# Kernel tuning notes

Hardware: AMD Instinct MI355X
Metric: run time of the kernel (lower is better)

The kernel has to match this reference:

```python
import jax, jax.numpy as jnp
import numpy as np

# Model dims
B, N, T = 2, 32, 256
D_MODEL = 128          # d_slow
D_STATE = 16
N_LAYERS = 2
EXPAND = 2
D_INNER = EXPAND * D_MODEL   # 256
D_CONV = 4
DT_RANK = (D_MODEL + 15) // 16  # 8


def setup_inputs() -> dict:
    key = jax.random.key(0)
    ks = jax.random.split(key, 8)
    s = lambda k, shape, scale: jax.random.normal(k, shape, jnp.float32) * scale
    return {
        "x": jax.random.normal(ks[0], (B, N, T, D_MODEL), jnp.float32),
        "in_proj_w": s(ks[1], (N_LAYERS, D_MODEL, 2 * D_INNER), 0.05),
        "conv_w": s(ks[2], (N_LAYERS, D_INNER, 1, D_CONV), 0.2),   # depthwise conv kernels
        "conv_b": jnp.zeros((N_LAYERS, D_INNER), jnp.float32),
        "x_proj_w": s(ks[3], (N_LAYERS, D_INNER, DT_RANK + 2 * D_STATE), 0.05),
        "dt_proj_w": s(ks[4], (N_LAYERS, DT_RANK, D_INNER), 0.1),
        "dt_proj_b": jnp.full((N_LAYERS, D_INNER), -4.0, jnp.float32),  # softplus(-4) ~ small dt
        # slow-timescale init: A_log = log(U(0.001, 0.1)) so A = -exp(A_log) is a weak decay
        "A_log": jnp.log(jax.random.uniform(ks[5], (N_LAYERS, D_INNER, D_STATE),
                                            minval=1e-3, maxval=0.1)),
        "D_param": jnp.ones((N_LAYERS, D_INNER), jnp.float32),
        "out_proj_w": s(ks[6], (N_LAYERS, D_INNER, D_MODEL), 0.05),
    }


def _selective_scan(u, delta, A, Bm, Cm, Dp):
    # u, delta: [b, t, d]; A: [d, n]; Bm, Cm: [b, t, n]; Dp: [d]
    deltaA = jnp.exp(jnp.einsum('btd,dn->btdn', delta, A))          # [b,t,d,n]
    deltaBu = jnp.einsum('btd,btn->btdn', delta * u, Bm)            # [b,t,d,n]
    # time-major for scan
    dA_t = jnp.transpose(deltaA, (1, 0, 2, 3))
    dBu_t = jnp.transpose(deltaBu, (1, 0, 2, 3))
    c_t = jnp.transpose(Cm, (1, 0, 2))

    def step(h, xs):
        dA, dBu, c = xs
        h = dA * h + dBu                                            # [b,d,n]
        y = jnp.einsum('bdn,bn->bd', h, c)
        return h, y

    h0 = jnp.zeros(u.shape[:1] + (u.shape[-1], A.shape[-1]), u.dtype)
    _, ys = jax.lax.scan(step, h0, (dA_t, dBu_t, c_t))              # ys: [t,b,d]
    y = jnp.transpose(ys, (1, 0, 2))
    return y + u * Dp


def _mamba_block(h, in_w, cw, cb, xw, dtw, dtb, A_log, Dp, ow):
    # h: [b, t, d_model]
    xz = h @ in_w                                                   # [b,t,2*d_inner]
    u, res = jnp.split(xz, 2, axis=-1)
    # causal depthwise conv over time
    u_nch = jnp.transpose(u, (0, 2, 1))                             # [b,d_inner,t]
    u_conv = jax.lax.conv_general_dilated(
        u_nch, cw, window_strides=(1,), padding=[(D_CONV - 1, 0)],
        dimension_numbers=('NCH', 'OIH', 'NCH'), feature_group_count=D_INNER)
    u = jax.nn.silu(jnp.transpose(u_conv + cb[None, :, None], (0, 2, 1)))
    # input-dependent dt, B, C
    dbl = u @ xw                                                    # [b,t,dt_rank+2n]
    dt, Bm, Cm = jnp.split(dbl, [DT_RANK, DT_RANK + D_STATE], axis=-1)
    delta = jax.nn.softplus(dt @ dtw + dtb)                         # [b,t,d_inner]
    A = -jnp.exp(A_log)                                             # [d_inner, n]
    y = _selective_scan(u, delta, A, Bm, Cm, Dp)
    return (y * jax.nn.silu(res)) @ ow


def reference(x, in_proj_w, conv_w, conv_b, x_proj_w, dt_proj_w, dt_proj_b,
              A_log, D_param, out_proj_w):
    b, n, t, d = x.shape
    h = x.reshape(b * n, t, d)
    for l in range(N_LAYERS):
        h = _mamba_block(h, in_proj_w[l], conv_w[l], conv_b[l], x_proj_w[l],
                         dt_proj_w[l], dt_proj_b[l], A_log[l], D_param[l],
                         out_proj_w[l])
    return h.reshape(b, n, t, d)
```

## Files before the change

### kernel.cpp

```cpp
#include <hip/hip_runtime.h>
#include <math.h>

#define BT 64
#define T 256
#define DM 128
#define DI 256
#define DS 16
#define DR 8
#define M_ROWS (BT*T)
#define NC 16
#define CL (T/NC)
#define SSZ (BT*DI*DS)

typedef __attribute__((ext_vector_type(8))) short short8v;
typedef __attribute__((ext_vector_type(4))) float f32x4;
typedef __attribute__((ext_vector_type(4))) unsigned int uint4v;
union U8 { unsigned int u[4]; uint4v v; short8v s; };

__device__ __forceinline__ float fast_silu(float x) {
  return x * __builtin_amdgcn_rcpf(1.0f + __expf(-x));
}
__device__ __forceinline__ float softplus_f(float x) {
  return fmaxf(x, 0.0f) + __logf(1.0f + __expf(-fabsf(x)));
}

__device__ __forceinline__ void split3(const float* x, short8v& o1, short8v& o2, short8v& o3) {
  unsigned int h1[8], h2[8], h3[8];
#pragma unroll
  for (int e = 0; e < 8; e++) {
    const float xe = x[e];
    const unsigned int a = __float_as_uint(xe) & 0xFFFF0000u;
    const float r1 = xe - __uint_as_float(a);
    const unsigned int b = __float_as_uint(r1) & 0xFFFF0000u;
    const float r2 = r1 - __uint_as_float(b);
    const unsigned int c = __float_as_uint(r2) & 0xFFFF0000u;
    h1[e] = a; h2[e] = b; h3[e] = c;
  }
  U8 u1, u2, u3;
#pragma unroll
  for (int q = 0; q < 4; q++) {
    u1.u[q] = (h1[2 * q] >> 16) | (h1[2 * q + 1] & 0xFFFF0000u);
    u2.u[q] = (h2[2 * q] >> 16) | (h2[2 * q + 1] & 0xFFFF0000u);
    u3.u[q] = (h3[2 * q] >> 16) | (h3[2 * q + 1] & 0xFFFF0000u);
  }
  o1 = u1.s; o2 = u2.s; o3 = u3.s;
}

__global__ __launch_bounds__(64) void prep_all(
    const float* __restrict__ in_w, const float* __restrict__ xw,
    const float* __restrict__ dtw, const float* __restrict__ ow,
    unsigned int* __restrict__ pw1, unsigned int* __restrict__ pwb,
    unsigned int* __restrict__ pow_) {
  const int b = blockIdx.x;
  const int l = threadIdx.x;
  const int rA = l & 15, kg = l >> 4;
  float x[8];
  unsigned int* dst;
  size_t base;
  if (b < 256) {
    const int layer = b >> 7, rem = b & 127;
    const int ks = rem >> 5, cf = rem & 31;
    const int col = cf * 16 + rA, k0 = ks * 32 + kg * 8;
    const float* W = in_w + (size_t)layer * 128 * 512;
#pragma unroll
    for (int e = 0; e < 8; e++) x[e] = W[(size_t)(k0 + e) * 512 + col];
    dst = pw1 + (size_t)layer * 98304;
    base = (((size_t)ks * 32 + cf) * 64 + l) * 4;
    short8v p1, p2, p3; split3(x, p1, p2, p3);
    U8 t;
    t.s = p1; *reinterpret_cast<uint4v*>(dst + base) = t.v;
    t.s = p2; *reinterpret_cast<uint4v*>(dst + 32768 + base) = t.v;
    t.s = p3; *reinterpret_cast<uint4v*>(dst + 65536 + base) = t.v;
  } else if (b < 576) {
    const int bb = b - 256;
    const int layer = bb / 160, rem = bb % 160;
    const int ks = rem / 20, cf = rem % 20;
    const int col = cf * 16 + rA, k0 = ks * 32 + kg * 8;
    const float* xwl = xw + (size_t)layer * DI * 40;
    const float* dtwl = dtw + (size_t)layer * DR * DI;
#pragma unroll
    for (int e = 0; e < 8; e++) {
      const int k = k0 + e;
      float v = 0.f;
      if (col < 256) {
#pragma unroll
        for (int r = 0; r < DR; r++) v += xwl[k * 40 + r] * dtwl[r * DI + col];
      } else if (col < 288) {
        v = xwl[k * 40 + 8 + (col - 256)];
      }
      x[e] = v;
    }
    dst = pwb + (size_t)layer * 122880;
    base = (((size_t)ks * 20 + cf) * 64 + l) * 4;
    short8v p1, p2, p3; split3(x, p1, p2, p3);
    U8 t;
    t.s = p1; *reinterpret_cast<uint4v*>(dst + base) = t.v;
    t.s = p2; *reinterpret_cast<uint4v*>(dst + 40960 + base) = t.v;
    t.s = p3; *reinterpret_cast<uint4v*>(dst + 81920 + base) = t.v;
  } else {
    const int bb = b - 576;
    const int layer = bb >> 6, rem = bb & 63;
    const int ks = rem >> 3, cf = rem & 7;
    const int col = cf * 16 + rA, k0 = ks * 32 + kg * 8;
    const float* W = ow + (size_t)layer * 256 * 128;
#pragma unroll
    for (int e = 0; e < 8; e++) x[e] = W[(size_t)(k0 + e) * 128 + col];
    dst = pow_ + (size_t)layer * 49152;
    base = (((size_t)ks * 8 + cf) * 64 + l) * 4;
    short8v p1, p2, p3; split3(x, p1, p2, p3);
    U8 t;
    t.s = p1; *reinterpret_cast<uint4v*>(dst + base) = t.v;
    t.s = p2; *reinterpret_cast<uint4v*>(dst + 16384 + base) = t.v;
    t.s = p3; *reinterpret_cast<uint4v*>(dst + 32768 + base) = t.v;
  }
}

template <int FR, int CF, int EPI>
__global__ __launch_bounds__(256, 4) void gemm_mfma(
    const float* __restrict__ Af, const unsigned int* __restrict__ Bp,
    float* __restrict__ C, float* __restrict__ Bb, float* __restrict__ Cb,
    const float* __restrict__ dtb, int M, int Nn, int K, int cpx) {
  const int NWC = Nn / (16 * CF);
  const int tile = (blockIdx.x & 7) * cpx + (blockIdx.x >> 3);
  const int wid = tile * 4 + (threadIdx.x >> 6);
  const int l = threadIdx.x & 63;
  const int mw = wid / NWC, nw = wid % NWC;
  const int wr0 = mw * (16 * FR), wc0 = nw * (16 * CF);
  const int rA = l & 15, kg = l >> 4;
  const int NF = Nn / 16, Kt = K >> 5;

  f32x4 acc[FR][CF];
#pragma unroll
  for (int fr = 0; fr < FR; fr++)
#pragma unroll
    for (int j = 0; j < CF; j++) acc[fr][j] = (f32x4){0.f, 0.f, 0.f, 0.f};

  for (int ks = 0; ks < Kt; ks++) {
    short8v bf[3][CF];
#pragma unroll
    for (int p = 0; p < 3; p++)
#pragma unroll
      for (int j = 0; j < CF; j++) {
        U8 t;
        t.v = *reinterpret_cast<const uint4v*>(
            Bp + ((((size_t)p * Kt + ks) * NF + (wc0 >> 4) + j) * 64 + l) * 4);
        bf[p][j] = t.s;
      }
#pragma unroll
    for (int fr = 0; fr < FR; fr++) {
      const float* ap = Af + (size_t)(wr0 + fr * 16 + rA) * K + ks * 32 + kg * 8;
      float x[8];
      *reinterpret_cast<float4*>(x) = *reinterpret_cast<const float4*>(ap);
      *reinterpret_cast<float4*>(x + 4) = *reinterpret_cast<const float4*>(ap + 4);
      short8v a1, a2, a3;
      split3(x, a1, a2, a3);
#pragma unroll
      for (int j = 0; j < CF; j++) {
        f32x4 c = acc[fr][j];
        c = __builtin_amdgcn_mfma_f32_16x16x32_bf16(a1, bf[0][j], c, 0, 0, 0);
        c = __builtin_amdgcn_mfma_f32_16x16x32_bf16(a1, bf[1][j], c, 0, 0, 0);
        c = __builtin_amdgcn_mfma_f32_16x16x32_bf16(a2, bf[0][j], c, 0, 0, 0);
        c = __builtin_amdgcn_mfma_f32_16x16x32_bf16(a1, bf[2][j], c, 0, 0, 0);
        c = __builtin_amdgcn_mfma_f32_16x16x32_bf16(a3, bf[0][j], c, 0, 0, 0);
        c = __builtin_amdgcn_mfma_f32_16x16x32_bf16(a2, bf[1][j], c, 0, 0, 0);
        acc[fr][j] = c;
      }
    }
  }

  const int cr = (l >> 4) * 4;
  const int cc = l & 15;
  if (EPI == 0) {
#pragma unroll
    for (int fr = 0; fr < FR; fr++)
#pragma unroll
      for (int j = 0; j < CF; j++) {
        const int col = wc0 + j * 16 + cc;
#pragma unroll
        for (int r = 0; r < 4; r++)
          C[(size_t)(wr0 + fr * 16 + cr + r) * Nn + col] = acc[fr][j][r];
      }
  } else if (EPI == 1) {
#pragma unroll
    for (int fr = 0; fr < FR; fr++)
#pragma unroll
      for (int j = 0; j < CF; j++) {
        const int col = wc0 + j * 16 + cc;
        if (col < 256) {
          const float bias = dtb[col];
#pragma unroll
          for (int r = 0; r < 4; r++)
            C[(size_t)(wr0 + fr * 16 + cr + r) * DI + col] =
                softplus_f(acc[fr][j][r] + bias);
        } else if (col < 272) {
#pragma unroll
          for (int r = 0; r < 4; r++)
            Bb[(size_t)(wr0 + fr * 16 + cr + r) * DS + (col - 256)] = acc[fr][j][r];
        } else if (col < 288) {
#pragma unroll
          for (int r = 0; r < 4; r++)
            Cb[(size_t)(wr0 + fr * 16 + cr + r) * DS + (col - 272)] = acc[fr][j][r];
        }
      }
  } else {
#pragma unroll
    for (int fr = 0; fr < FR; fr++)
#pragma unroll
      for (int j = 0; j < CF; j++) {
        const int col = wc0 + j * 16 + cc;
        if (col < 256) {
#pragma unroll
          for (int r = 0; r < 4; r++)
            C[(size_t)(wr0 + fr * 16 + cr + r) * Nn + col] = acc[fr][j][r];
        } else {
#pragma unroll
          for (int r = 0; r < 4; r++)
            C[(size_t)(wr0 + fr * 16 + cr + r) * Nn + col] = fast_silu(acc[fr][j][r]);
        }
      }
  }
}

__global__ __launch_bounds__(256) void conv_silu_kernel(
    const float* __restrict__ xzr,
    const float* __restrict__ cw, const float* __restrict__ cb,
    float* __restrict__ u) {
  const int d = threadIdx.x;
  const int m0 = blockIdx.x * 8;
  const int t0 = m0 & (T - 1);
  const float4 cv = *reinterpret_cast<const float4*>(&cw[d * 4]);
  const float bias = cb[d];
  float w0 = 0.f, w1 = 0.f, w2 = 0.f;
  if (t0 != 0) {
    w0 = xzr[(size_t)(m0 - 3) * 512 + d];
    w1 = xzr[(size_t)(m0 - 2) * 512 + d];
    w2 = xzr[(size_t)(m0 - 1) * 512 + d];
  }
#pragma unroll
  for (int i = 0; i < 8; i++) {
    const size_t m = m0 + i;
    const float cur = xzr[m * 512 + d];
    const float a = bias + cv.x * w0 + cv.y * w1 + cv.z * w2 + cv.w * cur;
    u[m * DI + d] = fast_silu(a);
    w0 = w1; w1 = w2; w2 = cur;
  }
}

__global__ __launch_bounds__(256) void scan_phase1(
    const float* __restrict__ delta, const float* __restrict__ u,
    const float* __restrict__ Bb, const float* __restrict__ A_log,
    float* __restrict__ Pb, float* __restrict__ H) {
  const int c  = blockIdx.x;
  const int bt = blockIdx.y;
  const int d  = threadIdx.x;

  float An[16];
  const float4* al = reinterpret_cast<const float4*>(&A_log[d * DS]);
#pragma unroll
  for (int q = 0; q < 4; q++) {
    float4 a = al[q];
    An[q * 4 + 0] = -__expf(a.x);
    An[q * 4 + 1] = -__expf(a.y);
    An[q * 4 + 2] = -__expf(a.z);
    An[q * 4 + 3] = -__expf(a.w);
  }

  float h[16];
#pragma unroll
  for (int n = 0; n < 16; n++) h[n] = 0.f;
  float Sdl = 0.f;

  const size_t m0 = (size_t)bt * T + c * CL;
  for (int t = 0; t < CL; t++) {
    const size_t m = m0 + t;
    const float dl = delta[m * DI + d];
    const float uu = u[m * DI + d];
    const float du = dl * uu;
    Sdl += dl;
    const float4* bp = reinterpret_cast<const float4*>(&Bb[m * DS]);
    const float4 B0 = bp[0], B1 = bp[1], B2 = bp[2], B3 = bp[3];
    const float Bv[16] = {B0.x, B0.y, B0.z, B0.w, B1.x, B1.y, B1.z, B1.w,
                          B2.x, B2.y, B2.z, B2.w, B3.x, B3.y, B3.z, B3.w};
#pragma unroll
    for (int n = 0; n < 16; n++) {
      const float dA = __expf(dl * An[n]);
      h[n] = dA * h[n] + du * Bv[n];
    }
  }

  const size_t idx = ((size_t)c * BT + bt) * 4096 + (size_t)d * 16;
#pragma unroll
  for (int q = 0; q < 4; q++) {
    float4 hv = {h[q * 4 + 0], h[q * 4 + 1], h[q * 4 + 2], h[q * 4 + 3]};
    *reinterpret_cast<float4*>(&H[idx + q * 4]) = hv;
  }
#pragma unroll
  for (int q = 0; q < 4; q++) {
    float4 pv = {__expf(An[q * 4 + 0] * Sdl), __expf(An[q * 4 + 1] * Sdl),
                 __expf(An[q * 4 + 2] * Sdl), __expf(An[q * 4 + 3] * Sdl)};
    *reinterpret_cast<float4*>(&Pb[idx + q * 4]) = pv;
  }
}

__global__ __launch_bounds__(256) void scan_phase2(
    const float* __restrict__ Pb, float* __restrict__ H) {
  const size_t i = (size_t)blockIdx.x * 256 + threadIdx.x;
  float hin = 0.f;
#pragma unroll
  for (int c = 0; c < NC; c++) {
    const size_t idx = (size_t)c * SSZ + i;
    const float Pv = Pb[idx];
    const float Hv = H[idx];
    H[idx] = hin;
    hin = Pv * hin + Hv;
  }
}

__global__ __launch_bounds__(256) void scan_phase3(
    const float* __restrict__ delta, const float* __restrict__ u,
    const float* __restrict__ Bb, const float* __restrict__ Cb,
    const float* __restrict__ xz,
    const float* __restrict__ A_log, const float* __restrict__ Dp,
    const float* __restrict__ H, float* __restrict__ g) {
  const int c  = blockIdx.x;
  const int bt = blockIdx.y;
  const int d  = threadIdx.x;

  float An[16];
  const float4* al = reinterpret_cast<const float4*>(&A_log[d * DS]);
#pragma unroll
  for (int q = 0; q < 4; q++) {
    float4 a = al[q];
    An[q * 4 + 0] = -__expf(a.x);
    An[q * 4 + 1] = -__expf(a.y);
    An[q * 4 + 2] = -__expf(a.z);
    An[q * 4 + 3] = -__expf(a.w);
  }
  const float Dpd = Dp[d];

  float h[16];
  const size_t idx = ((size_t)c * BT + bt) * 4096 + (size_t)d * 16;
#pragma unroll
  for (int q = 0; q < 4; q++) {
    float4 hv = *reinterpret_cast<const float4*>(&H[idx + q * 4]);
    h[q * 4 + 0] = hv.x; h[q * 4 + 1] = hv.y; h[q * 4 + 2] = hv.z; h[q * 4 + 3] = hv.w;
  }

  const size_t m0 = (size_t)bt * T + c * CL;
  for (int t = 0; t < CL; t++) {
    const size_t m = m0 + t;
    const float dl = delta[m * DI + d];
    const float uu = u[m * DI + d];
    const float du = dl * uu;
    const float4* bp = reinterpret_cast<const float4*>(&Bb[m * DS]);
    const float4 B0 = bp[0], B1 = bp[1], B2 = bp[2], B3 = bp[3];
    const float4* cp = reinterpret_cast<const float4*>(&Cb[m * DS]);
    const float4 C0 = cp[0], C1 = cp[1], C2 = cp[2], C3 = cp[3];
    const float Bv[16] = {B0.x, B0.y, B0.z, B0.w, B1.x, B1.y, B1.z, B1.w,
                          B2.x, B2.y, B2.z, B2.w, B3.x, B3.y, B3.z, B3.w};
    const float Cv[16] = {C0.x, C0.y, C0.z, C0.w, C1.x, C1.y, C1.z, C1.w,
                          C2.x, C2.y, C2.z, C2.w, C3.x, C3.y, C3.z, C3.w};
    float y = 0.f;
#pragma unroll
    for (int n = 0; n < 16; n++) {
      const float dA = __expf(dl * An[n]);
      h[n] = dA * h[n] + du * Bv[n];
      y += h[n] * Cv[n];
    }
    const float rs = xz[m * 512 + 256 + d];
    g[m * DI + d] = (y + uu * Dpd) * rs;
  }
}

extern "C" void kernel_launch(void* const* d_in, const int* in_sizes, int n_in,
                              void* d_out, int out_size, void* d_ws, size_t ws_size,
                              hipStream_t stream) {
  const float* x      = (const float*)d_in[0];
  const float* in_w   = (const float*)d_in[1];
  const float* conv_w = (const float*)d_in[2];
  const float* conv_b = (const float*)d_in[3];
  const float* xw     = (const float*)d_in[4];
  const float* dtw    = (const float*)d_in[5];
  const float* dtb    = (const float*)d_in[6];
  const float* A_log  = (const float*)d_in[7];
  const float* Dp     = (const float*)d_in[8];
  const float* ow     = (const float*)d_in[9];
  float* out = (float*)d_out;
  float* ws  = (float*)d_ws;

  float* xz = ws;
  float* u  = ws + 8388608;
  float* dg = ws + 12582912;
  float* Bb = ws + 16777216;
  float* Cb = ws + 17039360;
  float* hb = ws + 17301504;
  float* Hb = ws + 19398656;
  float* Pb = ws + 23592960;
  unsigned int* pl_w1 = (unsigned int*)(ws + 27787264);
  unsigned int* pl_wb = (unsigned int*)(ws + 27983872);
  unsigned int* pl_ow = (unsigned int*)(ws + 28229632);

  prep_all<<<704, 64, 0, stream>>>(in_w, xw, dtw, ow, pl_w1, pl_wb, pl_ow);

  for (int l = 0; l < 2; l++) {
    const float* Ain = (l == 0) ? x : hb;
    float* dst = (l == 1) ? out : hb;

    gemm_mfma<1, 4, 3><<<2048, 256, 0, stream>>>(
        Ain, pl_w1 + (size_t)l * 98304, xz,
        nullptr, nullptr, nullptr, M_ROWS, 512, 128, 256);

    conv_silu_kernel<<<M_ROWS / 8, 256, 0, stream>>>(
        xz, conv_w + (size_t)l * DI * 4, conv_b + (size_t)l * DI, u);

    gemm_mfma<1, 4, 1><<<1280, 256, 0, stream>>>(
        u, pl_wb + (size_t)l * 122880, dg, Bb, Cb, dtb + (size_t)l * DI,
        M_ROWS, 320, 256, 160);

    scan_phase1<<<dim3(NC, BT), 256, 0, stream>>>(
        dg, u, Bb, A_log + (size_t)l * DI * DS, Pb, Hb);

    scan_phase2<<<SSZ / 256, 256, 0, stream>>>(Pb, Hb);

    scan_phase3<<<dim3(NC, BT), 256, 0, stream>>>(
        dg, u, Bb, Cb, xz, A_log + (size_t)l * DI * DS, Dp + (size_t)l * DI,
        Hb, dg);

    gemm_mfma<1, 4, 0><<<512, 256, 0, stream>>>(
        dg, pl_ow + (size_t)l * 49152, dst, nullptr, nullptr, nullptr,
        M_ROWS, 128, 256, 64);
  }
}
```

Before: 256.4 us.

## Fuse three-phase chunked selective scan into one kernel using shared-memory carry propagation

The three scan kernels (per-chunk local scan, cross-chunk carry propagation, final output pass) are merged into one 1024-thread block per (sequence, 64-channel group). Chunk-end states and delta sums are exchanged through shared memory, and the carry pass runs in-block, so the global H/P intermediate buffers and two kernel launches per layer go away. In exchange, the grid shrinks to 256 large blocks, which may lower occupancy and latency hiding on the sequential scan loops. The shared-memory carry pass also adds two block-wide barriers.

```diff
diff --git a/kernel.cpp b/kernel.cpp
--- a/kernel.cpp
+++ b/kernel.cpp
@@ -10,7 +10,6 @@
 #define M_ROWS (BT*T)
 #define NC 16
 #define CL (T/NC)
-#define SSZ (BT*DI*DS)
 
 typedef __attribute__((ext_vector_type(8))) short short8v;
 typedef __attribute__((ext_vector_type(4))) float f32x4;
@@ -246,13 +245,20 @@
   }
 }
 
-__global__ __launch_bounds__(256) void scan_phase1(
+__global__ __launch_bounds__(1024) void scan_fused(
     const float* __restrict__ delta, const float* __restrict__ u,
-    const float* __restrict__ Bb, const float* __restrict__ A_log,
-    float* __restrict__ Pb, float* __restrict__ H) {
-  const int c  = blockIdx.x;
-  const int bt = blockIdx.y;
-  const int d  = threadIdx.x;
+    const float* __restrict__ Bb, const float* __restrict__ Cb,
+    const float* __restrict__ xz,
+    const float* __restrict__ A_log, const float* __restrict__ Dp,
+    float* __restrict__ g) {
+  __shared__ float sH[DS][NC][64];
+  __shared__ float sS[NC][64];
+  const int bt = blockIdx.x;
+  const int dq = blockIdx.y;
+  const int tid = threadIdx.x;
+  const int c  = tid >> 6;
+  const int dl = tid & 63;
+  const int d  = dq * 64 + dl;
 
   float An[16];
   const float4* al = reinterpret_cast<const float4*>(&A_log[d * DS]);
@@ -273,85 +279,50 @@
   const size_t m0 = (size_t)bt * T + c * CL;
   for (int t = 0; t < CL; t++) {
     const size_t m = m0 + t;
-    const float dl = delta[m * DI + d];
+    const float dlv = delta[m * DI + d];
     const float uu = u[m * DI + d];
-    const float du = dl * uu;
-    Sdl += dl;
+    const float du = dlv * uu;
+    Sdl += dlv;
     const float4* bp = reinterpret_cast<const float4*>(&Bb[m * DS]);
     const float4 B0 = bp[0], B1 = bp[1], B2 = bp[2], B3 = bp[3];
     const float Bv[16] = {B0.x, B0.y, B0.z, B0.w, B1.x, B1.y, B1.z, B1.w,
                           B2.x, B2.y, B2.z, B2.w, B3.x, B3.y, B3.z, B3.w};
 #pragma unroll
     for (int n = 0; n < 16; n++) {
-      const float dA = __expf(dl * An[n]);
+      const float dA = __expf(dlv * An[n]);
       h[n] = dA * h[n] + du * Bv[n];
     }
   }
-
-  const size_t idx = ((size_t)c * BT + bt) * 4096 + (size_t)d * 16;
-#pragma unroll
-  for (int q = 0; q < 4; q++) {
-    float4 hv = {h[q * 4 + 0], h[q * 4 + 1], h[q * 4 + 2], h[q * 4 + 3]};
-    *reinterpret_cast<float4*>(&H[idx + q * 4]) = hv;
-  }
-#pragma unroll
-  for (int q = 0; q < 4; q++) {
-    float4 pv = {__expf(An[q * 4 + 0] * Sdl), __expf(An[q * 4 + 1] * Sdl),
-                 __expf(An[q * 4 + 2] * Sdl), __expf(An[q * 4 + 3] * Sdl)};
-    *reinterpret_cast<float4*>(&Pb[idx + q * 4]) = pv;
-  }
-}
-
-__global__ __launch_bounds__(256) void scan_phase2(
-    const float* __restrict__ Pb, float* __restrict__ H) {
-  const size_t i = (size_t)blockIdx.x * 256 + threadIdx.x;
-  float hin = 0.f;
-#pragma unroll
-  for (int c = 0; c < NC; c++) {
-    const size_t idx = (size_t)c * SSZ + i;
-    const float Pv = Pb[idx];
-    const float Hv = H[idx];
-    H[idx] = hin;
-    hin = Pv * hin + Hv;
-  }
-}
-
-__global__ __launch_bounds__(256) void scan_phase3(
-    const float* __restrict__ delta, const float* __restrict__ u,
-    const float* __restrict__ Bb, const float* __restrict__ Cb,
-    const float* __restrict__ xz,
-    const float* __restrict__ A_log, const float* __restrict__ Dp,
-    const float* __restrict__ H, float* __restrict__ g) {
-  const int c  = blockIdx.x;
-  const int bt = blockIdx.y;
-  const int d  = threadIdx.x;
-
-  float An[16];
-  const float4* al = reinterpret_cast<const float4*>(&A_log[d * DS]);
-#pragma unroll
-  for (int q = 0; q < 4; q++) {
-    float4 a = al[q];
-    An[q * 4 + 0] = -__expf(a.x);
-    An[q * 4 + 1] = -__expf(a.y);
-    An[q * 4 + 2] = -__expf(a.z);
-    An[q * 4 + 3] = -__expf(a.w);
-  }
+#pragma unroll
+  for (int n = 0; n < 16; n++) sH[n][c][dl] = h[n];
+  sS[c][dl] = Sdl;
+  __syncthreads();
+
+  {
+    const int n2 = tid >> 6;
+    const int dl2 = tid & 63;
+    const int d2 = dq * 64 + dl2;
+    const float An2 = -__expf(A_log[d2 * DS + n2]);
+    float hin = 0.f;
+#pragma unroll
+    for (int cc = 0; cc < NC; cc++) {
+      const float sdl = sS[cc][dl2];
+      const float Hv = sH[n2][cc][dl2];
+      sH[n2][cc][dl2] = hin;
+      hin = __expf(An2 * sdl) * hin + Hv;
+    }
+  }
+  __syncthreads();
+
+#pragma unroll
+  for (int n = 0; n < 16; n++) h[n] = sH[n][c][dl];
   const float Dpd = Dp[d];
 
-  float h[16];
-  const size_t idx = ((size_t)c * BT + bt) * 4096 + (size_t)d * 16;
-#pragma unroll
-  for (int q = 0; q < 4; q++) {
-    float4 hv = *reinterpret_cast<const float4*>(&H[idx + q * 4]);
-    h[q * 4 + 0] = hv.x; h[q * 4 + 1] = hv.y; h[q * 4 + 2] = hv.z; h[q * 4 + 3] = hv.w;
-  }
-
-  const size_t m0 = (size_t)bt * T + c * CL;
   for (int t = 0; t < CL; t++) {
     const size_t m = m0 + t;
-    const float dl = delta[m * DI + d];
+    const float dlv = delta[m * DI + d];
     const float uu = u[m * DI + d];
-    const float du = dl * uu;
+    const float du = dlv * uu;
     const float4* bp = reinterpret_cast<const float4*>(&Bb[m * DS]);
     const float4 B0 = bp[0], B1 = bp[1], B2 = bp[2], B3 = bp[3];
     const float4* cp = reinterpret_cast<const float4*>(&Cb[m * DS]);
@@ -363,7 +334,7 @@
     float y = 0.f;
 #pragma unroll
     for (int n = 0; n < 16; n++) {
-      const float dA = __expf(dl * An[n]);
+      const float dA = __expf(dlv * An[n]);
       h[n] = dA * h[n] + du * Bv[n];
       y += h[n] * Cv[n];
     }
@@ -394,8 +365,6 @@
   float* Bb = ws + 16777216;
   float* Cb = ws + 17039360;
   float* hb = ws + 17301504;
-  float* Hb = ws + 19398656;
-  float* Pb = ws + 23592960;
   unsigned int* pl_w1 = (unsigned int*)(ws + 27787264);
   unsigned int* pl_wb = (unsigned int*)(ws + 27983872);
   unsigned int* pl_ow = (unsigned int*)(ws + 28229632);
@@ -417,14 +386,9 @@
         u, pl_wb + (size_t)l * 122880, dg, Bb, Cb, dtb + (size_t)l * DI,
         M_ROWS, 320, 256, 160);
 
-    scan_phase1<<<dim3(NC, BT), 256, 0, stream>>>(
-        dg, u, Bb, A_log + (size_t)l * DI * DS, Pb, Hb);
-
-    scan_phase2<<<SSZ / 256, 256, 0, stream>>>(Pb, Hb);
-
-    scan_phase3<<<dim3(NC, BT), 256, 0, stream>>>(
+    scan_fused<<<dim3(BT, 4), 1024, 0, stream>>>(
         dg, u, Bb, Cb, xz, A_log + (size_t)l * DI * DS, Dp + (size_t)l * DI,
-        Hb, dg);
+        dg);
 
     gemm_mfma<1, 4, 0><<<512, 256, 0, stream>>>(
         dg, pl_ow + (size_t)l * 49152, dst, nullptr, nullptr, nullptr,
```

Measured after the change: 226.0 us. 11.9% less time.
